# Optimization experiments

Hardware: AMD Instinct MI355X
Metric: run time of the kernel (lower is better)

Reference implementation:

```python
import jax, jax.numpy as jnp
import numpy as np

R = 3                 # corr_radius
STRIDE = 4
RES = (384, 512)      # model_resolution (H, W)
G = 2 * R + 1         # 7: support grid side


def setup_inputs() -> dict:
    key = jax.random.key(0)
    ks = jax.random.split(key, 16)
    B, S, N, C = 1, 8, 1024, 128
    H0, W0 = RES[0] // STRIDE, RES[1] // STRIDE  # 96, 128
    inp = {}
    for i in range(4):
        h, w = H0 >> i, W0 >> i
        inp[f"fmaps{i}"] = jax.random.normal(ks[i], (B, S, C, h, w), jnp.float32)
        inp[f"track{i}"] = jax.random.normal(ks[4 + i], (B, G * G, N, C), jnp.float32)
    inp["coords"] = jax.random.uniform(ks[8], (B, S, N, 2), jnp.float32) * jnp.asarray([W0 - 1.0, H0 - 1.0], jnp.float32)
    inp["vis"] = jax.random.normal(ks[9], (B, S, N, 1), jnp.float32)
    inp["conf"] = jax.random.normal(ks[10], (B, S, N, 1), jnp.float32)
    r2 = G * G
    inp["w1"] = jax.random.normal(ks[11], (r2 * r2, 384), jnp.float32) * (1.0 / np.sqrt(r2 * r2))
    inp["b1"] = jnp.zeros((384,), jnp.float32)
    inp["w2"] = jax.random.normal(ks[12], (384, 256), jnp.float32) * (1.0 / np.sqrt(384))
    inp["b2"] = jnp.zeros((256,), jnp.float32)
    inp["time_emb"] = jax.random.normal(ks[13], (1, S, 1110), jnp.float32) * 0.02
    return inp


def bilinear_sample(fmap, x, y):
    """fmap: (BT, C, H, W); x, y: (BT, M) pixel coords. Border padding, align_corners=True
    (matches torch grid_sample as used by co-tracker's bilinear_sampler)."""
    BT, C, H, W = fmap.shape
    x0f = jnp.floor(x)
    y0f = jnp.floor(y)
    wx = (x - x0f)[:, None, :]
    wy = (y - y0f)[:, None, :]
    x0 = jnp.clip(x0f.astype(jnp.int32), 0, W - 1)
    x1 = jnp.clip(x0f.astype(jnp.int32) + 1, 0, W - 1)
    y0 = jnp.clip(y0f.astype(jnp.int32), 0, H - 1)
    y1 = jnp.clip(y0f.astype(jnp.int32) + 1, 0, H - 1)
    flat = fmap.reshape(BT, C, H * W)

    def g(yi, xi):
        idx = (yi * W + xi)[:, None, :]  # (BT, 1, M)
        return jnp.take_along_axis(flat, idx, axis=2)  # (BT, C, M)

    return (g(y0, x0) * (1 - wx) * (1 - wy) + g(y0, x1) * wx * (1 - wy)
            + g(y1, x0) * (1 - wx) * wy + g(y1, x1) * wx * wy)


def posenc(x, min_deg=0, max_deg=10):
    scales = jnp.asarray([2.0 ** i for i in range(min_deg, max_deg)], x.dtype)
    xb = (x[..., None, :] * scales[:, None]).reshape(x.shape[:-1] + (-1,))
    four = jnp.sin(jnp.concatenate([xb, xb + 0.5 * jnp.pi], axis=-1))
    return jnp.concatenate([x, four], axis=-1)


def reference(fmaps0, fmaps1, fmaps2, fmaps3, track0, track1, track2, track3,
              coords, vis, conf, w1, b1, w2, b2, time_emb):
    B, S, N, _ = coords.shape
    fps = [fmaps0, fmaps1, fmaps2, fmaps3]
    tps = [track0, track1, track2, track3]
    d = jnp.linspace(-R, R, G)
    xoff, yoff = jnp.meshgrid(d, d, indexing='ij')  # (7,7): rows = x offset, cols = y offset

    embs = []
    for lvl in range(4):
        fm = fps[lvl]
        C, H, W = fm.shape[2], fm.shape[3], fm.shape[4]
        c = coords.reshape(B * S, N, 1, 1, 2) / (2.0 ** lvl)
        x = c[..., 0] + xoff          # (B*S, N, 7, 7)
        y = c[..., 1] + yoff
        M = N * G * G
        sampled = bilinear_sample(fm.reshape(B * S, C, H, W), x.reshape(B * S, M), y.reshape(B * S, M))
        corr_feat = sampled.reshape(B, S, C, N, G, G).transpose(0, 1, 3, 4, 5, 2)  # (B,S,N,7,7,C)
        track = tps[lvl].reshape(B, G, G, N, C).transpose(0, 3, 1, 2, 4)           # (B,N,7,7,C)
        vol = jnp.einsum('btnhwc,bnijc->btnhwij', corr_feat, track)                # (B,S,N,7,7,7,7)
        h = jax.nn.gelu(vol.reshape(B * S * N, G * G * G * G) @ w1 + b1, approximate=False)
        embs.append(h @ w2 + b2)
    corr_embs = jnp.concatenate(embs, axis=-1).reshape(B, S, N, -1)  # (B,S,N,1024)

    rel_f = jnp.pad(coords[:, :-1] - coords[:, 1:], ((0, 0), (0, 1), (0, 0), (0, 0)))
    rel_b = jnp.pad(coords[:, 1:] - coords[:, :-1], ((0, 0), (1, 0), (0, 0), (0, 0)))
    scale = jnp.asarray([RES[1], RES[0]], jnp.float32) / STRIDE
    rel_emb = posenc(jnp.concatenate([rel_f / scale, rel_b / scale], axis=-1))  # (B,S,N,84)

    x = jnp.concatenate([vis, conf, corr_embs, rel_emb], axis=-1)  # (B,S,N,1110)
    x = x.transpose(0, 2, 1, 3).reshape(B * N, S, -1) + time_emb
    return x.reshape(B, N, S, -1)
```

## Files before the change

kernel.cpp:

```cpp
#include <hip/hip_runtime.h>
#include <math.h>


#define SN 8
#define NN 1024
#define CC 128
#define K1P 2432
#define H1 384
#define H2 256
#define DOUT 1110

typedef short bf16x8 __attribute__((ext_vector_type(8)));
typedef float f32x4 __attribute__((ext_vector_type(4)));

__device__ inline unsigned short f2b(float x) {
    union { float f; unsigned u; } v; v.f = x;
    unsigned r = v.u + 0x7FFFu + ((v.u >> 16) & 1u);
    return (unsigned short)(r >> 16);
}
__device__ inline float b2f(unsigned short u) {
    union { unsigned u; float f; } v; v.u = (unsigned)u << 16; return v.f;
}
__device__ inline void gll16(const void* g, void* l) {
    __builtin_amdgcn_global_load_lds(
        (const __attribute__((address_space(1))) void*)g,
        (__attribute__((address_space(3))) void*)l, 16, 0, 0);
}
__device__ inline int swz(int row, int g) {
    return row * 128 + ((g ^ (row & 7)) << 3);
}

__global__ __launch_bounds__(256) void conv_fmap_kernel(
    const float* __restrict__ in, unsigned short* __restrict__ outp,
    int H, int W)
{
    const int Hp = H + 8, Wp = W + 8;
    const int s = blockIdx.x / Hp, yp = blockIdx.x % Hp;
    const int y = min(max(yp - 4, 0), H - 1);
    const float* src = in + (size_t)s * CC * H * W + (size_t)y * W;
    unsigned short* dst = outp + ((size_t)s * Hp + yp) * Wp * CC;
    for (int idx = threadIdx.x; idx < Wp * CC; idx += 256) {
        int xp = idx >> 7, c = idx & 127;
        int x = min(max(xp - 4, 0), W - 1);
        dst[idx] = f2b(src[(size_t)c * H * W + x]);
    }
}

__global__ __launch_bounds__(256, 2) void sample_vol_kernel(
    const unsigned short* __restrict__ fpad,
    const float* __restrict__ track,
    const float* __restrict__ coords,
    unsigned short* __restrict__ vol,
    int Hp, int Wp, int lvl)
{
    __shared__ __align__(16) unsigned short patch[80 * 128];
    __shared__ __align__(16) unsigned short trk[64 * 128];
    __shared__ __align__(16) float pcL[80 * 68];
    const int n = blockIdx.x, t = threadIdx.x;
    const int lane = t & 63, wv = t >> 6;
    const int rsub = lane & 15, kq = lane >> 4;
    const float inv = 1.0f / (float)(1 << lvl);
    const size_t plane = (size_t)Hp * Wp * CC;

    int poff[5], ldso[5];
    #pragma unroll
    for (int i = 0; i < 5; ++i) {
        int task64 = wv * 5 + i;
        int point = task64 * 4 + (lane >> 4);
        int v = point / 10, xs = point - v * 10;
        int j = (lane & 15) ^ (point & 7);
        poff[i] = (v * Wp + xs) * CC + j * 8;
        ldso[i] = task64 * 512;
    }

    float cx = coords[((size_t)0 * NN + n) * 2 + 0] * inv;
    float cy = coords[((size_t)0 * NN + n) * 2 + 1] * inv;
    int fx = (int)floorf(cx), fy = (int)floorf(cy);
    int e = (fx - 3) & ~1;
    {
        const unsigned short* base =
            fpad + ((fy + 1) * Wp + (e + 4)) * CC;
        #pragma unroll
        for (int i = 0; i < 5; ++i) gll16(base + poff[i], &patch[ldso[i]]);
    }
    for (int task = t; task < 49 * 16; task += 256) {
        int row = task >> 4, g = task & 15;
        const float* srcp = &track[((size_t)row * NN + n) * CC + g * 8];
        float4 f0 = *(const float4*)srcp;
        float4 f1 = *(const float4*)(srcp + 4);
        bf16x8 v8;
        v8[0] = f2b(f0.x); v8[1] = f2b(f0.y); v8[2] = f2b(f0.z); v8[3] = f2b(f0.w);
        v8[4] = f2b(f1.x); v8[5] = f2b(f1.y); v8[6] = f2b(f1.z); v8[7] = f2b(f1.w);
        *(bf16x8*)&trk[swz(row, g)] = v8;
    }

    for (int sl = 0; sl < SN; ++sl) {
        const float wx = cx - (float)fx, wy = cy - (float)fy;
        const float w00 = (1.f - wx) * (1.f - wy), w10 = wx * (1.f - wy);
        const float w01 = (1.f - wx) * wy,         w11 = wx * wy;
        const int off = fx - 3 - e;

        asm volatile("s_waitcnt vmcnt(0)" ::: "memory");
        __syncthreads();

        {
            f32x4 acc[5] = {};
            #pragma unroll
            for (int kk = 0; kk < 4; ++kk) {
                int gg = kk * 4 + kq;
                bf16x8 b = *(const bf16x8*)&trk[swz(wv * 16 + rsub, gg)];
                #pragma unroll
                for (int ti = 0; ti < 5; ++ti) {
                    int row = ti * 16 + rsub;
                    bf16x8 a = *(const bf16x8*)&patch[swz(row, gg)];
                    acc[ti] = __builtin_amdgcn_mfma_f32_16x16x32_bf16(a, b, acc[ti], 0, 0, 0);
                }
            }
            #pragma unroll
            for (int ti = 0; ti < 5; ++ti)
                #pragma unroll
                for (int r = 0; r < 4; ++r)
                    pcL[(ti * 16 + kq * 4 + r) * 68 + wv * 16 + rsub] = acc[ti][r];
        }
        __syncthreads();

        if (sl + 1 < SN) {
            int s2 = sl + 1;
            cx = coords[((size_t)s2 * NN + n) * 2 + 0] * inv;
            cy = coords[((size_t)s2 * NN + n) * 2 + 1] * inv;
            fx = (int)floorf(cx); fy = (int)floorf(cy);
            e = (fx - 3) & ~1;
            const unsigned short* base =
                fpad + (size_t)s2 * plane + ((fy + 1) * Wp + (e + 4)) * CC;
            #pragma unroll
            for (int i = 0; i < 5; ++i) gll16(base + poff[i], &patch[ldso[i]]);
        }

        {
            unsigned* vrow32 = (unsigned*)(vol + ((size_t)sl * NN + n) * K1P);
            for (int d = t; d < K1P / 2; d += 256) {
                int s0 = 2 * d;
                unsigned pk = 0;
                if (s0 < 2401) {
                    int ab0 = s0 / 49, ij0 = s0 - 49 * ab0;
                    int a0 = ab0 / 7, b0 = ab0 - 7 * a0;
                    int p0 = b0 * 10 + off + a0;
                    const float* q = &pcL[p0 * 68 + ij0];
                    float v0 = w00 * q[0] + w10 * q[68] + w01 * q[680] + w11 * q[748];
                    unsigned short lo = f2b(v0), hi = 0;
                    int s1 = s0 + 1;
                    if (s1 < 2401) {
                        int ab1 = ab0, ij1 = ij0 + 1;
                        if (ij1 == 49) { ij1 = 0; ab1 = ab0 + 1; }
                        int a1 = ab1 / 7, b1 = ab1 - 7 * a1;
                        int p1 = b1 * 10 + off + a1;
                        const float* q1 = &pcL[p1 * 68 + ij1];
                        float v1 = w00 * q1[0] + w10 * q1[68] + w01 * q1[680] + w11 * q1[748];
                        hi = f2b(v1);
                    }
                    pk = (unsigned)lo | ((unsigned)hi << 16);
                }
                vrow32[d] = pk;
            }
        }
    }
}

__global__ __launch_bounds__(256) void gemm1_kernel(
    const unsigned short* __restrict__ A,
    const unsigned short* __restrict__ Bt,
    const float* __restrict__ bias,
    unsigned short* __restrict__ Hout)
{
    __shared__ __align__(16) unsigned short As[2][128 * 32];
    __shared__ __align__(16) unsigned short Bs[2][128 * 32];
    const int h = blockIdx.x, q = gridDim.x >> 3;
    const int l = (h & 7) * q + (h >> 3);
    const int m0 = (l / 3) * 128, n0 = (l % 3) * 128;
    const int t = threadIdx.x, lane = t & 63, wv = t >> 6;
    const int wm = wv >> 1, wn = wv & 1;
    const int rsub = lane & 15, kq = lane >> 4;

    const int rA0 = t >> 2, sA0 = (t & 3) ^ ((rA0 >> 1) & 3);
    const int rA1 = (t + 256) >> 2, sA1 = ((t + 256) & 3) ^ ((rA1 >> 1) & 3);
    const unsigned short* gA0 = A  + (size_t)(m0 + rA0) * K1P + sA0 * 8;
    const unsigned short* gA1 = A  + (size_t)(m0 + rA1) * K1P + sA1 * 8;
    const unsigned short* gB0 = Bt + (size_t)(n0 + rA0) * K1P + sA0 * 8;
    const unsigned short* gB1 = Bt + (size_t)(n0 + rA1) * K1P + sA1 * 8;
    const int chunk0 = (t & ~63) * 8, chunk1 = (256 + (t & ~63)) * 8;

    f32x4 acc[4][4] = {};

    const int NSTEP = K1P / 32;
    {
        gll16(gA0, &As[0][chunk0]); gll16(gA1, &As[0][chunk1]);
        gll16(gB0, &Bs[0][chunk0]); gll16(gB1, &Bs[0][chunk1]);
        gll16(gA0 + 32, &As[1][chunk0]); gll16(gA1 + 32, &As[1][chunk1]);
        gll16(gB0 + 32, &Bs[1][chunk0]); gll16(gB1 + 32, &Bs[1][chunk1]);
    }
    for (int st = 0; st < NSTEP; ++st) {
        const int cur = st & 1;
        asm volatile("s_waitcnt vmcnt(4)" ::: "memory");
        __builtin_amdgcn_s_barrier();
        __builtin_amdgcn_sched_barrier(0);
        bf16x8 af[4], bfr[4];
        #pragma unroll
        for (int mi = 0; mi < 4; ++mi) {
            int r = wm * 64 + mi * 16 + rsub;
            int phys = r * 4 + (kq ^ ((r >> 1) & 3));
            af[mi] = *(const bf16x8*)&As[cur][phys * 8];
        }
        #pragma unroll
        for (int ni = 0; ni < 4; ++ni) {
            int r = wn * 64 + ni * 16 + rsub;
            int phys = r * 4 + (kq ^ ((r >> 1) & 3));
            bfr[ni] = *(const bf16x8*)&Bs[cur][phys * 8];
        }
        #pragma unroll
        for (int mi = 0; mi < 4; ++mi)
            #pragma unroll
            for (int ni = 0; ni < 4; ++ni)
                acc[mi][ni] = __builtin_amdgcn_mfma_f32_16x16x32_bf16(
                    af[mi], bfr[ni], acc[mi][ni], 0, 0, 0);
        __builtin_amdgcn_sched_barrier(0);
        __builtin_amdgcn_s_barrier();
        __builtin_amdgcn_sched_barrier(0);
        if (st + 2 < NSTEP) {
            size_t ko = (size_t)(st + 2) * 32;
            gll16(gA0 + ko, &As[cur][chunk0]);
            gll16(gA1 + ko, &As[cur][chunk1]);
            gll16(gB0 + ko, &Bs[cur][chunk0]);
            gll16(gB1 + ko, &Bs[cur][chunk1]);
        }
    }
    #pragma unroll
    for (int mi = 0; mi < 4; ++mi) {
        int row = m0 + wm * 64 + mi * 16 + kq * 4;
        #pragma unroll
        for (int ni = 0; ni < 4; ++ni) {
            int col = n0 + wn * 64 + ni * 16 + rsub;
            float bcol = bias[col];
            #pragma unroll
            for (int r = 0; r < 4; ++r) {
                float x = acc[mi][ni][r] + bcol;
                float g = 0.5f * x * (1.f + erff(x * 0.70710678118654752f));
                Hout[(size_t)(row + r) * H1 + col] = f2b(g);
            }
        }
    }
}

__global__ __launch_bounds__(256) void gemm2_kernel(
    const unsigned short* __restrict__ A,
    const unsigned short* __restrict__ Bt,
    const float* __restrict__ bias,
    const float* __restrict__ te,
    float* __restrict__ out,
    int lv0)
{
    __shared__ __align__(16) unsigned short As[2][128 * 32];
    __shared__ __align__(16) unsigned short Bs[2][128 * 32];
    const int h = blockIdx.x, q = gridDim.x >> 3;
    const int l = (h & 7) * q + (h >> 3);
    const int m0 = (l >> 1) * 128, n0 = (l & 1) * 128;
    const int t = threadIdx.x, lane = t & 63, wv = t >> 6;
    const int wm = wv >> 1, wn = wv & 1;
    const int rsub = lane & 15, kq = lane >> 4;

    const int rA0 = t >> 2, sA0 = (t & 3) ^ ((rA0 >> 1) & 3);
    const int rA1 = (t + 256) >> 2, sA1 = ((t + 256) & 3) ^ ((rA1 >> 1) & 3);
    const unsigned short* gA0 = A  + (size_t)(m0 + rA0) * H1 + sA0 * 8;
    const unsigned short* gA1 = A  + (size_t)(m0 + rA1) * H1 + sA1 * 8;
    const unsigned short* gB0 = Bt + (size_t)(n0 + rA0) * H1 + sA0 * 8;
    const unsigned short* gB1 = Bt + (size_t)(n0 + rA1) * H1 + sA1 * 8;
    const int chunk0 = (t & ~63) * 8, chunk1 = (256 + (t & ~63)) * 8;

    f32x4 acc[4][4] = {};

    const int NSTEP = H1 / 32;
    {
        gll16(gA0, &As[0][chunk0]); gll16(gA1, &As[0][chunk1]);
        gll16(gB0, &Bs[0][chunk0]); gll16(gB1, &Bs[0][chunk1]);
        gll16(gA0 + 32, &As[1][chunk0]); gll16(gA1 + 32, &As[1][chunk1]);
        gll16(gB0 + 32, &Bs[1][chunk0]); gll16(gB1 + 32, &Bs[1][chunk1]);
    }
    for (int st = 0; st < NSTEP; ++st) {
        const int cur = st & 1;
        asm volatile("s_waitcnt vmcnt(4)" ::: "memory");
        __builtin_amdgcn_s_barrier();
        __builtin_amdgcn_sched_barrier(0);
        bf16x8 af[4], bfr[4];
        #pragma unroll
        for (int mi = 0; mi < 4; ++mi) {
            int r = wm * 64 + mi * 16 + rsub;
            int phys = r * 4 + (kq ^ ((r >> 1) & 3));
            af[mi] = *(const bf16x8*)&As[cur][phys * 8];
        }
        #pragma unroll
        for (int ni = 0; ni < 4; ++ni) {
            int r = wn * 64 + ni * 16 + rsub;
            int phys = r * 4 + (kq ^ ((r >> 1) & 3));
            bfr[ni] = *(const bf16x8*)&Bs[cur][phys * 8];
        }
        #pragma unroll
        for (int mi = 0; mi < 4; ++mi)
            #pragma unroll
            for (int ni = 0; ni < 4; ++ni)
                acc[mi][ni] = __builtin_amdgcn_mfma_f32_16x16x32_bf16(
                    af[mi], bfr[ni], acc[mi][ni], 0, 0, 0);
        __builtin_amdgcn_sched_barrier(0);
        __builtin_amdgcn_s_barrier();
        __builtin_amdgcn_sched_barrier(0);
        if (st + 2 < NSTEP) {
            size_t ko = (size_t)(st + 2) * 32;
            gll16(gA0 + ko, &As[cur][chunk0]);
            gll16(gA1 + ko, &As[cur][chunk1]);
            gll16(gB0 + ko, &Bs[cur][chunk0]);
            gll16(gB1 + ko, &Bs[cur][chunk1]);
        }
    }
    #pragma unroll
    for (int mi = 0; mi < 4; ++mi) {
        int rowb = m0 + wm * 64 + mi * 16 + kq * 4;
        #pragma unroll
        for (int ni = 0; ni < 4; ++ni) {
            int col = n0 + wn * 64 + ni * 16 + rsub;
            float bcol = bias[col];
            #pragma unroll
            for (int r = 0; r < 4; ++r) {
                int row = rowb + r;
                int g = row >> 13, s = (row >> 10) & 7, n = row & 1023;
                int dcol = 2 + (lv0 + g) * H2 + col;
                out[((size_t)n * SN + s) * DOUT + dcol] =
                    acc[mi][ni][r] + bcol + te[s * DOUT + dcol];
            }
        }
    }
}

__global__ __launch_bounds__(256) void conv_t_kernel(
    const float* __restrict__ in, unsigned short* __restrict__ outp,
    int K, int Nw, int Kp)
{
    __shared__ float tile[32][33];
    const int kb = blockIdx.x * 32, nb = blockIdx.y * 32;
    const int tx = threadIdx.x & 31, ty = threadIdx.x >> 5;
    #pragma unroll
    for (int i = 0; i < 32; i += 8) {
        int k = kb + ty + i, nn = nb + tx;
        tile[ty + i][tx] = (k < K && nn < Nw) ? in[(size_t)k * Nw + nn] : 0.f;
    }
    __syncthreads();
    #pragma unroll
    for (int i = 0; i < 32; i += 8) {
        int nn = nb + ty + i, k = kb + tx;
        if (nn < Nw) outp[(size_t)nn * Kp + k] = f2b(tile[tx][ty + i]);
    }
}

__global__ __launch_bounds__(128) void tail_kernel(
    const float* __restrict__ coords, const float* __restrict__ vis,
    const float* __restrict__ conf, const float* __restrict__ te,
    float* __restrict__ out)
{
    const int b = blockIdx.x;
    const int n = b >> 3, s = b & 7;
    const int d = threadIdx.x;
    if (d >= 86) return;
    const size_t ob = (size_t)b * DOUT;
    if (d == 0) {
        out[ob + 0] = vis[(size_t)s * NN + n] + te[s * DOUT + 0];
    } else if (d == 1) {
        out[ob + 1] = conf[(size_t)s * NN + n] + te[s * DOUT + 1];
    } else {
        int rd = d - 2;
        float cx = coords[((size_t)s * NN + n) * 2 + 0];
        float cy = coords[((size_t)s * NN + n) * 2 + 1];
        float rfx = 0.f, rfy = 0.f, rbx = 0.f, rby = 0.f;
        if (s < SN - 1) {
            rfx = cx - coords[((size_t)(s + 1) * NN + n) * 2 + 0];
            rfy = cy - coords[((size_t)(s + 1) * NN + n) * 2 + 1];
        }
        if (s > 0) {
            rbx = cx - coords[((size_t)(s - 1) * NN + n) * 2 + 0];
            rby = cy - coords[((size_t)(s - 1) * NN + n) * 2 + 1];
        }
        float r4[4] = {rfx / 128.f, rfy / 96.f, rbx / 128.f, rby / 96.f};
        float val;
        if (rd < 4) {
            val = r4[rd];
        } else if (rd < 44) {
            int q = rd - 4; int deg = q >> 2, comp = q & 3;
            val = sinf(r4[comp] * (float)(1 << deg));
        } else {
            int q = rd - 44; int deg = q >> 2, comp = q & 3;
            val = sinf(r4[comp] * (float)(1 << deg) + 1.57079632679489662f);
        }
        int od = 1026 + rd;
        out[ob + od] = val + te[s * DOUT + od];
    }
}

extern "C" void kernel_launch(void* const* d_in, const int* in_sizes, int n_in,
                              void* d_out, int out_size, void* d_ws, size_t ws_size,
                              hipStream_t stream) {
    const float* fmaps[4] = {(const float*)d_in[0], (const float*)d_in[2],
                             (const float*)d_in[4], (const float*)d_in[6]};
    const float* track[4] = {(const float*)d_in[1], (const float*)d_in[3],
                             (const float*)d_in[5], (const float*)d_in[7]};
    const float* coords = (const float*)d_in[8];
    const float* vis    = (const float*)d_in[9];
    const float* conf   = (const float*)d_in[10];
    const float* w1     = (const float*)d_in[11];
    const float* b1     = (const float*)d_in[12];
    const float* w2     = (const float*)d_in[13];
    const float* b2     = (const float*)d_in[14];
    const float* te     = (const float*)d_in[15];
    float* out = (float*)d_out;

    const int Hs[4] = {96, 48, 24, 12};
    const int Ws[4] = {128, 64, 32, 16};

    char* wsb = (char*)d_ws;
    unsigned short* w1t = (unsigned short*)wsb;
    size_t off = (size_t)H1 * K1P * 2;
    unsigned short* w2t = (unsigned short*)(wsb + off);
    off += (size_t)H2 * H1 * 2;
    unsigned short* fpad[4];
    for (int l = 0; l < 4; ++l) {
        fpad[l] = (unsigned short*)(wsb + off);
        off += (size_t)SN * (Hs[l] + 8) * (Ws[l] + 8) * CC * 2;
    }
    off += 512;
    const size_t fixed = off;
    int n_lv = 4;
    while (n_lv > 1 &&
           fixed + (size_t)n_lv * SN * NN * (K1P + H1) * 2 > ws_size)
        n_lv >>= 1;
    unsigned short* volb = (unsigned short*)(wsb + fixed);
    unsigned short* hb   = volb + (size_t)n_lv * SN * NN * K1P;

    conv_t_kernel<<<dim3(K1P / 32, H1 / 32), 256, 0, stream>>>(w1, w1t, 2401, H1, K1P);
    conv_t_kernel<<<dim3(H1 / 32, H2 / 32), 256, 0, stream>>>(w2, w2t, H1, H2, H1);
    for (int l = 0; l < 4; ++l)
        conv_fmap_kernel<<<SN * (Hs[l] + 8), 256, 0, stream>>>(
            fmaps[l], fpad[l], Hs[l], Ws[l]);

    for (int lv0 = 0; lv0 < 4; lv0 += n_lv) {
        for (int g = 0; g < n_lv; ++g) {
            int l = lv0 + g;
            sample_vol_kernel<<<NN, 256, 0, stream>>>(
                fpad[l], track[l], coords, volb + (size_t)g * SN * NN * K1P,
                Hs[l] + 8, Ws[l] + 8, l);
        }
        const int rows = n_lv * SN * NN;
        gemm1_kernel<<<(rows / 128) * 3, 256, 0, stream>>>(volb, w1t, b1, hb);
        gemm2_kernel<<<(rows / 128) * 2, 256, 0, stream>>>(hb, w2t, b2, te, out, lv0);
    }
    tail_kernel<<<SN * NN, 128, 0, stream>>>(coords, vis, conf, te, out);
}
```

Before: 409.4 us.

## Merge per-level sampling launches, store corr in bf16, triple-buffer GEMM pipelines

Replaces the per-level sample_vol launches with one launch covering all levels in a group, selecting the feature map and track pointers by block index. The sampling kernel now preloads all coordinates, precomputes index tables for the volume gather, stores the correlation patch in LDS as bf16 to cut LDS size, and raises occupancy to 3 blocks per CU. Both GEMM kernels switch from double to triple buffering with a deeper prefetch distance and adjusted vmcnt waits. The bf16 intermediate adds rounding error, and the extra LDS and registers may limit occupancy.

```diff
diff --git a/kernel.cpp b/kernel.cpp
--- a/kernel.cpp
+++ b/kernel.cpp
@@ -46,21 +46,30 @@
     }
 }
 
-__global__ __launch_bounds__(256, 2) void sample_vol_kernel(
-    const unsigned short* __restrict__ fpad,
-    const float* __restrict__ track,
+__global__ __launch_bounds__(256, 3) void sample_vol_kernel(
+    const unsigned short* __restrict__ fq0, const unsigned short* __restrict__ fq1,
+    const unsigned short* __restrict__ fq2, const unsigned short* __restrict__ fq3,
+    const float* __restrict__ tk0, const float* __restrict__ tk1,
+    const float* __restrict__ tk2, const float* __restrict__ tk3,
     const float* __restrict__ coords,
     unsigned short* __restrict__ vol,
-    int Hp, int Wp, int lvl)
+    int lv0)
 {
     __shared__ __align__(16) unsigned short patch[80 * 128];
     __shared__ __align__(16) unsigned short trk[64 * 128];
-    __shared__ __align__(16) float pcL[80 * 68];
-    const int n = blockIdx.x, t = threadIdx.x;
+    __shared__ __align__(16) unsigned short pcL[80 * 66];
+    const int n = blockIdx.x & 1023, g = blockIdx.x >> 10;
+    const int lvl = lv0 + g;
+    const unsigned short* fpad = (lvl == 0) ? fq0 : (lvl == 1) ? fq1
+                               : (lvl == 2) ? fq2 : fq3;
+    const float* track = (lvl == 0) ? tk0 : (lvl == 1) ? tk1
+                       : (lvl == 2) ? tk2 : tk3;
+    const int Wp = (128 >> lvl) + 8;
+    const int t = threadIdx.x;
     const int lane = t & 63, wv = t >> 6;
     const int rsub = lane & 15, kq = lane >> 4;
     const float inv = 1.0f / (float)(1 << lvl);
-    const size_t plane = (size_t)Hp * Wp * CC;
+    const size_t plane = (size_t)((96 >> lvl) + 8) * Wp * CC;
 
     int poff[5], ldso[5];
     #pragma unroll
@@ -73,32 +82,53 @@
         ldso[i] = task64 * 512;
     }
 
-    float cx = coords[((size_t)0 * NN + n) * 2 + 0] * inv;
-    float cy = coords[((size_t)0 * NN + n) * 2 + 1] * inv;
-    int fx = (int)floorf(cx), fy = (int)floorf(cy);
+    float cxa[SN], cya[SN];
+    #pragma unroll
+    for (int s = 0; s < SN; ++s) {
+        float2 c2 = *(const float2*)&coords[((size_t)s * NN + n) * 2];
+        cxa[s] = c2.x * inv; cya[s] = c2.y * inv;
+    }
+
+    unsigned lutA[5], lutB[5];
+    #pragma unroll
+    for (int i = 0; i < 5; ++i) {
+        int d = t + i * 256;
+        int o0 = 2 * d, o1 = 2 * d + 1;
+        lutA[i] = 0xFFFFFFFFu; lutB[i] = 0xFFFFFFFFu;
+        if (o0 < 2401) {
+            int ab = o0 / 49, ij = o0 - 49 * ab, a = ab / 7, b = ab - 7 * a;
+            lutA[i] = (unsigned)((b * 10 + a) * 66 + ij);
+        }
+        if (o1 < 2401) {
+            int ab = o1 / 49, ij = o1 - 49 * ab, a = ab / 7, b = ab - 7 * a;
+            lutB[i] = (unsigned)((b * 10 + a) * 66 + ij);
+        }
+    }
+
+    int fx = (int)floorf(cxa[0]), fy = (int)floorf(cya[0]);
     int e = (fx - 3) & ~1;
     {
-        const unsigned short* base =
-            fpad + ((fy + 1) * Wp + (e + 4)) * CC;
+        const unsigned short* base = fpad + ((fy + 1) * Wp + (e + 4)) * CC;
         #pragma unroll
         for (int i = 0; i < 5; ++i) gll16(base + poff[i], &patch[ldso[i]]);
     }
     for (int task = t; task < 49 * 16; task += 256) {
-        int row = task >> 4, g = task & 15;
-        const float* srcp = &track[((size_t)row * NN + n) * CC + g * 8];
+        int row = task >> 4, gg = task & 15;
+        const float* srcp = &track[((size_t)row * NN + n) * CC + gg * 8];
         float4 f0 = *(const float4*)srcp;
         float4 f1 = *(const float4*)(srcp + 4);
         bf16x8 v8;
         v8[0] = f2b(f0.x); v8[1] = f2b(f0.y); v8[2] = f2b(f0.z); v8[3] = f2b(f0.w);
         v8[4] = f2b(f1.x); v8[5] = f2b(f1.y); v8[6] = f2b(f1.z); v8[7] = f2b(f1.w);
-        *(bf16x8*)&trk[swz(row, g)] = v8;
-    }
-
+        *(bf16x8*)&trk[swz(row, gg)] = v8;
+    }
+
+    #pragma unroll
     for (int sl = 0; sl < SN; ++sl) {
-        const float wx = cx - (float)fx, wy = cy - (float)fy;
+        const float wx = cxa[sl] - (float)fx, wy = cya[sl] - (float)fy;
         const float w00 = (1.f - wx) * (1.f - wy), w10 = wx * (1.f - wy);
         const float w01 = (1.f - wx) * wy,         w11 = wx * wy;
-        const int off = fx - 3 - e;
+        const int offs = (fx - 3 - e) * 66;
 
         asm volatile("s_waitcnt vmcnt(0)" ::: "memory");
         __syncthreads();
@@ -111,69 +141,62 @@
                 bf16x8 b = *(const bf16x8*)&trk[swz(wv * 16 + rsub, gg)];
                 #pragma unroll
                 for (int ti = 0; ti < 5; ++ti) {
-                    int row = ti * 16 + rsub;
-                    bf16x8 a = *(const bf16x8*)&patch[swz(row, gg)];
+                    bf16x8 a = *(const bf16x8*)&patch[swz(ti * 16 + rsub, gg)];
                     acc[ti] = __builtin_amdgcn_mfma_f32_16x16x32_bf16(a, b, acc[ti], 0, 0, 0);
                 }
             }
+            const int col = wv * 16 + rsub;
             #pragma unroll
             for (int ti = 0; ti < 5; ++ti)
                 #pragma unroll
                 for (int r = 0; r < 4; ++r)
-                    pcL[(ti * 16 + kq * 4 + r) * 68 + wv * 16 + rsub] = acc[ti][r];
+                    pcL[(ti * 16 + kq * 4 + r) * 66 + col] = f2b(acc[ti][r]);
         }
         __syncthreads();
 
         if (sl + 1 < SN) {
-            int s2 = sl + 1;
-            cx = coords[((size_t)s2 * NN + n) * 2 + 0] * inv;
-            cy = coords[((size_t)s2 * NN + n) * 2 + 1] * inv;
-            fx = (int)floorf(cx); fy = (int)floorf(cy);
+            fx = (int)floorf(cxa[sl + 1]); fy = (int)floorf(cya[sl + 1]);
             e = (fx - 3) & ~1;
             const unsigned short* base =
-                fpad + (size_t)s2 * plane + ((fy + 1) * Wp + (e + 4)) * CC;
+                fpad + (size_t)(sl + 1) * plane + ((fy + 1) * Wp + (e + 4)) * CC;
             #pragma unroll
             for (int i = 0; i < 5; ++i) gll16(base + poff[i], &patch[ldso[i]]);
         }
 
         {
-            unsigned* vrow32 = (unsigned*)(vol + ((size_t)sl * NN + n) * K1P);
-            for (int d = t; d < K1P / 2; d += 256) {
-                int s0 = 2 * d;
-                unsigned pk = 0;
-                if (s0 < 2401) {
-                    int ab0 = s0 / 49, ij0 = s0 - 49 * ab0;
-                    int a0 = ab0 / 7, b0 = ab0 - 7 * a0;
-                    int p0 = b0 * 10 + off + a0;
-                    const float* q = &pcL[p0 * 68 + ij0];
-                    float v0 = w00 * q[0] + w10 * q[68] + w01 * q[680] + w11 * q[748];
-                    unsigned short lo = f2b(v0), hi = 0;
-                    int s1 = s0 + 1;
-                    if (s1 < 2401) {
-                        int ab1 = ab0, ij1 = ij0 + 1;
-                        if (ij1 == 49) { ij1 = 0; ab1 = ab0 + 1; }
-                        int a1 = ab1 / 7, b1 = ab1 - 7 * a1;
-                        int p1 = b1 * 10 + off + a1;
-                        const float* q1 = &pcL[p1 * 68 + ij1];
-                        float v1 = w00 * q1[0] + w10 * q1[68] + w01 * q1[680] + w11 * q1[748];
-                        hi = f2b(v1);
+            unsigned* vrow32 = (unsigned*)(vol + ((size_t)(g * SN + sl) * NN + n) * K1P);
+            #pragma unroll
+            for (int i = 0; i < 5; ++i) {
+                int d = t + i * 256;
+                if (d < K1P / 2) {
+                    unsigned lo = 0, hi = 0;
+                    if (lutA[i] != 0xFFFFFFFFu) {
+                        int idx = (int)lutA[i] + offs;
+                        float v = w00 * b2f(pcL[idx])       + w10 * b2f(pcL[idx + 66])
+                                + w01 * b2f(pcL[idx + 660]) + w11 * b2f(pcL[idx + 726]);
+                        lo = f2b(v);
                     }
-                    pk = (unsigned)lo | ((unsigned)hi << 16);
+                    if (lutB[i] != 0xFFFFFFFFu) {
+                        int idx = (int)lutB[i] + offs;
+                        float v = w00 * b2f(pcL[idx])       + w10 * b2f(pcL[idx + 66])
+                                + w01 * b2f(pcL[idx + 660]) + w11 * b2f(pcL[idx + 726]);
+                        hi = f2b(v);
+                    }
+                    vrow32[d] = lo | (hi << 16);
                 }
-                vrow32[d] = pk;
             }
         }
     }
 }
 
-__global__ __launch_bounds__(256) void gemm1_kernel(
+__global__ __launch_bounds__(256, 3) void gemm1_kernel(
     const unsigned short* __restrict__ A,
     const unsigned short* __restrict__ Bt,
     const float* __restrict__ bias,
     unsigned short* __restrict__ Hout)
 {
-    __shared__ __align__(16) unsigned short As[2][128 * 32];
-    __shared__ __align__(16) unsigned short Bs[2][128 * 32];
+    __shared__ __align__(16) unsigned short As[3 * 128 * 32];
+    __shared__ __align__(16) unsigned short Bs[3 * 128 * 32];
     const int h = blockIdx.x, q = gridDim.x >> 3;
     const int l = (h & 7) * q + (h >> 3);
     const int m0 = (l / 3) * 128, n0 = (l % 3) * 128;
@@ -192,29 +215,34 @@
     f32x4 acc[4][4] = {};
 
     const int NSTEP = K1P / 32;
-    {
-        gll16(gA0, &As[0][chunk0]); gll16(gA1, &As[0][chunk1]);
-        gll16(gB0, &Bs[0][chunk0]); gll16(gB1, &Bs[0][chunk1]);
-        gll16(gA0 + 32, &As[1][chunk0]); gll16(gA1 + 32, &As[1][chunk1]);
-        gll16(gB0 + 32, &Bs[1][chunk0]); gll16(gB1 + 32, &Bs[1][chunk1]);
-    }
+    #pragma unroll
+    for (int p = 0; p < 3; ++p) {
+        size_t ko = (size_t)p * 32;
+        int lb = p * 4096;
+        gll16(gA0 + ko, &As[lb + chunk0]); gll16(gA1 + ko, &As[lb + chunk1]);
+        gll16(gB0 + ko, &Bs[lb + chunk0]); gll16(gB1 + ko, &Bs[lb + chunk1]);
+    }
+    int cur = 0;
     for (int st = 0; st < NSTEP; ++st) {
-        const int cur = st & 1;
-        asm volatile("s_waitcnt vmcnt(4)" ::: "memory");
+        const int rem = NSTEP - 1 - st;
+        if (rem >= 2)      asm volatile("s_waitcnt vmcnt(8)" ::: "memory");
+        else if (rem == 1) asm volatile("s_waitcnt vmcnt(4)" ::: "memory");
+        else               asm volatile("s_waitcnt vmcnt(0)" ::: "memory");
         __builtin_amdgcn_s_barrier();
         __builtin_amdgcn_sched_barrier(0);
+        const int lb = cur * 4096;
         bf16x8 af[4], bfr[4];
         #pragma unroll
         for (int mi = 0; mi < 4; ++mi) {
             int r = wm * 64 + mi * 16 + rsub;
             int phys = r * 4 + (kq ^ ((r >> 1) & 3));
-            af[mi] = *(const bf16x8*)&As[cur][phys * 8];
+            af[mi] = *(const bf16x8*)&As[lb + phys * 8];
         }
         #pragma unroll
         for (int ni = 0; ni < 4; ++ni) {
             int r = wn * 64 + ni * 16 + rsub;
             int phys = r * 4 + (kq ^ ((r >> 1) & 3));
-            bfr[ni] = *(const bf16x8*)&Bs[cur][phys * 8];
+            bfr[ni] = *(const bf16x8*)&Bs[lb + phys * 8];
         }
         #pragma unroll
         for (int mi = 0; mi < 4; ++mi)
@@ -225,13 +253,14 @@
         __builtin_amdgcn_sched_barrier(0);
         __builtin_amdgcn_s_barrier();
         __builtin_amdgcn_sched_barrier(0);
-        if (st + 2 < NSTEP) {
-            size_t ko = (size_t)(st + 2) * 32;
-            gll16(gA0 + ko, &As[cur][chunk0]);
-            gll16(gA1 + ko, &As[cur][chunk1]);
-            gll16(gB0 + ko, &Bs[cur][chunk0]);
-            gll16(gB1 + ko, &Bs[cur][chunk1]);
-        }
+        if (st + 3 < NSTEP) {
+            size_t ko = (size_t)(st + 3) * 32;
+            gll16(gA0 + ko, &As[lb + chunk0]);
+            gll16(gA1 + ko, &As[lb + chunk1]);
+            gll16(gB0 + ko, &Bs[lb + chunk0]);
+            gll16(gB1 + ko, &Bs[lb + chunk1]);
+        }
+        cur = (cur == 2) ? 0 : cur + 1;
     }
     #pragma unroll
     for (int mi = 0; mi < 4; ++mi) {
@@ -243,14 +272,14 @@
             #pragma unroll
             for (int r = 0; r < 4; ++r) {
                 float x = acc[mi][ni][r] + bcol;
-                float g = 0.5f * x * (1.f + erff(x * 0.70710678118654752f));
-                Hout[(size_t)(row + r) * H1 + col] = f2b(g);
+                float gg = 0.5f * x * (1.f + erff(x * 0.70710678118654752f));
+                Hout[(size_t)(row + r) * H1 + col] = f2b(gg);
             }
         }
     }
 }
 
-__global__ __launch_bounds__(256) void gemm2_kernel(
+__global__ __launch_bounds__(256, 3) void gemm2_kernel(
     const unsigned short* __restrict__ A,
     const unsigned short* __restrict__ Bt,
     const float* __restrict__ bias,
@@ -258,8 +287,8 @@
     float* __restrict__ out,
     int lv0)
 {
-    __shared__ __align__(16) unsigned short As[2][128 * 32];
-    __shared__ __align__(16) unsigned short Bs[2][128 * 32];
+    __shared__ __align__(16) unsigned short As[3 * 128 * 32];
+    __shared__ __align__(16) unsigned short Bs[3 * 128 * 32];
     const int h = blockIdx.x, q = gridDim.x >> 3;
     const int l = (h & 7) * q + (h >> 3);
     const int m0 = (l >> 1) * 128, n0 = (l & 1) * 128;
@@ -278,29 +307,34 @@
     f32x4 acc[4][4] = {};
 
     const int NSTEP = H1 / 32;
-    {
-        gll16(gA0, &As[0][chunk0]); gll16(gA1, &As[0][chunk1]);
-        gll16(gB0, &Bs[0][chunk0]); gll16(gB1, &Bs[0][chunk1]);
-        gll16(gA0 + 32, &As[1][chunk0]); gll16(gA1 + 32, &As[1][chunk1]);
-        gll16(gB0 + 32, &Bs[1][chunk0]); gll16(gB1 + 32, &Bs[1][chunk1]);
-    }
+    #pragma unroll
+    for (int p = 0; p < 3; ++p) {
+        size_t ko = (size_t)p * 32;
+        int lb = p * 4096;
+        gll16(gA0 + ko, &As[lb + chunk0]); gll16(gA1 + ko, &As[lb + chunk1]);
+        gll16(gB0 + ko, &Bs[lb + chunk0]); gll16(gB1 + ko, &Bs[lb + chunk1]);
+    }
+    int cur = 0;
     for (int st = 0; st < NSTEP; ++st) {
-        const int cur = st & 1;
-        asm volatile("s_waitcnt vmcnt(4)" ::: "memory");
+        const int rem = NSTEP - 1 - st;
+        if (rem >= 2)      asm volatile("s_waitcnt vmcnt(8)" ::: "memory");
+        else if (rem == 1) asm volatile("s_waitcnt vmcnt(4)" ::: "memory");
+        else               asm volatile("s_waitcnt vmcnt(0)" ::: "memory");
         __builtin_amdgcn_s_barrier();
         __builtin_amdgcn_sched_barrier(0);
+        const int lb = cur * 4096;
         bf16x8 af[4], bfr[4];
         #pragma unroll
         for (int mi = 0; mi < 4; ++mi) {
             int r = wm * 64 + mi * 16 + rsub;
             int phys = r * 4 + (kq ^ ((r >> 1) & 3));
-            af[mi] = *(const bf16x8*)&As[cur][phys * 8];
+            af[mi] = *(const bf16x8*)&As[lb + phys * 8];
         }
         #pragma unroll
         for (int ni = 0; ni < 4; ++ni) {
             int r = wn * 64 + ni * 16 + rsub;
             int phys = r * 4 + (kq ^ ((r >> 1) & 3));
-            bfr[ni] = *(const bf16x8*)&Bs[cur][phys * 8];
+            bfr[ni] = *(const bf16x8*)&Bs[lb + phys * 8];
         }
         #pragma unroll
         for (int mi = 0; mi < 4; ++mi)
@@ -311,13 +345,14 @@
         __builtin_amdgcn_sched_barrier(0);
         __builtin_amdgcn_s_barrier();
         __builtin_amdgcn_sched_barrier(0);
-        if (st + 2 < NSTEP) {
-            size_t ko = (size_t)(st + 2) * 32;
-            gll16(gA0 + ko, &As[cur][chunk0]);
-            gll16(gA1 + ko, &As[cur][chunk1]);
-            gll16(gB0 + ko, &Bs[cur][chunk0]);
-            gll16(gB1 + ko, &Bs[cur][chunk1]);
-        }
+        if (st + 3 < NSTEP) {
+            size_t ko = (size_t)(st + 3) * 32;
+            gll16(gA0 + ko, &As[lb + chunk0]);
+            gll16(gA1 + ko, &As[lb + chunk1]);
+            gll16(gB0 + ko, &Bs[lb + chunk0]);
+            gll16(gB1 + ko, &Bs[lb + chunk1]);
+        }
+        cur = (cur == 2) ? 0 : cur + 1;
     }
     #pragma unroll
     for (int mi = 0; mi < 4; ++mi) {
@@ -447,12 +482,10 @@
             fmaps[l], fpad[l], Hs[l], Ws[l]);
 
     for (int lv0 = 0; lv0 < 4; lv0 += n_lv) {
-        for (int g = 0; g < n_lv; ++g) {
-            int l = lv0 + g;
-            sample_vol_kernel<<<NN, 256, 0, stream>>>(
-                fpad[l], track[l], coords, volb + (size_t)g * SN * NN * K1P,
-                Hs[l] + 8, Ws[l] + 8, l);
-        }
+        sample_vol_kernel<<<n_lv * NN, 256, 0, stream>>>(
+            fpad[0], fpad[1], fpad[2], fpad[3],
+            track[0], track[1], track[2], track[3],
+            coords, volb, lv0);
         const int rows = n_lv * SN * NN;
         gemm1_kernel<<<(rows / 128) * 3, 256, 0, stream>>>(volb, w1t, b1, hb);
         gemm2_kernel<<<(rows / 128) * 2, 256, 0, stream>>>(hb, w2t, b2, te, out, lv0);
```

Result: faster. 347.5 us (-15.1%).
